# Kernel optimization log

Hardware: AMD Instinct MI355X
Metric: run time of the kernel (lower is better)

Reference implementation:

```python
import jax, jax.numpy as jnp
import numpy as np

DIM = 1024
HEADS = 16
HEAD_DIM = DIM // HEADS
THRESH = 0.29514
SHARP = 15.0
LN_EPS = 1e-5
NORM_EPS = 1e-12


def setup_inputs() -> dict:
    key = jax.random.key(0)
    ks = jax.random.split(key, 8)
    s = 1.0 / np.sqrt(DIM)
    sg = 1.0 / np.sqrt(HEAD_DIM)
    return {
        "x": jax.random.normal(ks[0], (2, 2048, DIM), dtype=jnp.float32),
        "Wq": jax.random.uniform(ks[1], (DIM, DIM), jnp.float32, -s, s),
        "Wk": jax.random.uniform(ks[2], (DIM, DIM), jnp.float32, -s, s),
        "Wv": jax.random.uniform(ks[3], (DIM, DIM), jnp.float32, -s, s),
        "gq": jax.random.uniform(ks[4], (HEAD_DIM,), jnp.float32, -sg, sg),
        "gk": jax.random.uniform(ks[5], (HEAD_DIM,), jnp.float32, -sg, sg),
        "Wo": jax.random.uniform(ks[6], (DIM, DIM), jnp.float32, -s, s),
        "bo": jax.random.uniform(ks[7], (DIM,), jnp.float32, -s, s),
        "ln_w": jnp.ones((DIM,), jnp.float32),
        "ln_b": jnp.zeros((DIM,), jnp.float32),
    }


def _l2norm(t):
    # F.normalize: t / max(||t||_2, eps)
    n = jnp.sqrt(jnp.sum(t * t, axis=-1, keepdims=True))
    return t / jnp.maximum(n, NORM_EPS)


def reference(x, Wq, Wk, Wv, gq, gk, Wo, bo, ln_w, ln_b):
    B, T, D = x.shape
    # LayerNorm over last dim
    mu = jnp.mean(x, axis=-1, keepdims=True)
    var = jnp.mean((x - mu) ** 2, axis=-1, keepdims=True)
    x_norm = (x - mu) / jnp.sqrt(var + LN_EPS) * ln_w + ln_b

    def split_heads(t):  # [B,T,D] -> [B,H,T,hd]
        return t.reshape(B, T, HEADS, HEAD_DIM).transpose(0, 2, 1, 3)

    q = _l2norm(split_heads(x_norm @ Wq))
    k = _l2norm(split_heads(x_norm @ Wk))
    v = split_heads(x @ Wv)  # note: v uses un-normalized x, as in source

    align = jnp.einsum("bhtd,bhsd->bhts", q, k)  # cosine alignment
    resonance = jax.nn.sigmoid((align - THRESH) * SHARP)
    gate_q = jnp.einsum("bhtd,d->bht", q, gq)
    gate_k = jnp.einsum("bhsd,d->bhs", k, gk)
    modulation = resonance * gate_q[..., :, None] * gate_k[..., None, :]
    collapse = jnp.einsum("bhts,bhsd->bhtd", modulation, v)
    collapse = collapse.transpose(0, 2, 1, 3).reshape(B, T, D)
    return collapse @ Wo + bo
```

## Files before the change

kernel.cpp:

```cpp
#include <hip/hip_runtime.h>
#include <math.h>

#define DIM 1024
#define T_SEQ 2048
#define NBATCH 2
#define HEADS 16
#define HD 64
#define NTOK 4096
#define THRESH 0.29514f
#define SHARP 15.0f
#define LOG2E 1.4426950408889634f

typedef __attribute__((ext_vector_type(8))) short bf16x8;
typedef __attribute__((ext_vector_type(4))) float f32x4;
typedef __attribute__((ext_vector_type(4))) unsigned int u32x4;

__device__ __forceinline__ unsigned short f2b(float f) {
    unsigned int u = __float_as_uint(f);
    unsigned int r = (u + 0x7FFFu + ((u >> 16) & 1u)) >> 16;
    return (unsigned short)r;
}
__device__ __forceinline__ float b2f(unsigned short u) {
    return __uint_as_float(((unsigned int)u) << 16);
}
__device__ __forceinline__ unsigned int pack2_bf16(float lo, float hi) {
    unsigned int a = __float_as_uint(lo) + 0x8000u;
    unsigned int b = __float_as_uint(hi) + 0x8000u;
    return __builtin_amdgcn_perm(b, a, 0x07060302u);
}

__device__ __forceinline__ void async_cp16(const unsigned short* g, unsigned short* l) {
    __builtin_amdgcn_global_load_lds(
        (const __attribute__((address_space(1))) unsigned int*)g,
        (__attribute__((address_space(3))) unsigned int*)l, 16, 0, 0);
}

__global__ __launch_bounds__(256) void ln_xnorm_kernel(
    const float* __restrict__ x, const float* __restrict__ lnw, const float* __restrict__ lnb,
    unsigned short* __restrict__ xnb, unsigned short* __restrict__ xb) {
    int row = blockIdx.x * 4 + (threadIdx.x >> 6);
    int lane = threadIdx.x & 63;
    const float4* xr = (const float4*)(x + (size_t)row * DIM);
    float4 v[4];
    float s = 0.f, ss = 0.f;
#pragma unroll
    for (int i = 0; i < 4; i++) {
        v[i] = xr[lane + i * 64];
        s += v[i].x + v[i].y + v[i].z + v[i].w;
        ss += v[i].x * v[i].x + v[i].y * v[i].y + v[i].z * v[i].z + v[i].w * v[i].w;
    }
#pragma unroll
    for (int off = 32; off; off >>= 1) {
        s += __shfl_xor(s, off);
        ss += __shfl_xor(ss, off);
    }
    float m = s * (1.f / DIM);
    float rstd = rsqrtf(ss * (1.f / DIM) - m * m + 1e-5f);
#pragma unroll
    for (int i = 0; i < 4; i++) {
        int e = (lane + i * 64) * 4;
        float4 lw = *(const float4*)&lnw[e];
        float4 lb = *(const float4*)&lnb[e];
        ushort4 un, ur;
        un.x = f2b((v[i].x - m) * rstd * lw.x + lb.x);
        un.y = f2b((v[i].y - m) * rstd * lw.y + lb.y);
        un.z = f2b((v[i].z - m) * rstd * lw.z + lb.z);
        un.w = f2b((v[i].w - m) * rstd * lw.w + lb.w);
        ur.x = f2b(v[i].x); ur.y = f2b(v[i].y); ur.z = f2b(v[i].z); ur.w = f2b(v[i].w);
        *(ushort4*)&xnb[(size_t)row * DIM + e] = un;
        *(ushort4*)&xb[(size_t)row * DIM + e] = ur;
    }
}

__global__ __launch_bounds__(256) void wtrans_kernel(
    const float* __restrict__ W0, const float* __restrict__ W1,
    const float* __restrict__ W2, const float* __restrict__ W3,
    unsigned short* __restrict__ T0, unsigned short* __restrict__ T1,
    unsigned short* __restrict__ T2, unsigned short* __restrict__ T3) {
    __shared__ float tile[64][65];
    const int z = blockIdx.z;
    const float* W = (z == 0) ? W0 : (z == 1) ? W1 : (z == 2) ? W2 : W3;
    unsigned short* T = (z == 0) ? T0 : (z == 1) ? T1 : (z == 2) ? T2 : T3;
    const int k0 = blockIdx.x * 64, n0 = blockIdx.y * 64;
    const int r = threadIdx.x >> 3;
    const int c = (threadIdx.x & 7) * 8;
#pragma unroll
    for (int half = 0; half < 2; half++) {
        int rr = r + half * 32;
        float4 a = *(const float4*)&W[(size_t)(k0 + rr) * DIM + n0 + c];
        float4 b = *(const float4*)&W[(size_t)(k0 + rr) * DIM + n0 + c + 4];
        tile[rr][c + 0] = a.x; tile[rr][c + 1] = a.y; tile[rr][c + 2] = a.z; tile[rr][c + 3] = a.w;
        tile[rr][c + 4] = b.x; tile[rr][c + 5] = b.y; tile[rr][c + 6] = b.z; tile[rr][c + 7] = b.w;
    }
    __syncthreads();
#pragma unroll
    for (int half = 0; half < 2; half++) {
        int dd = r + half * 32;
        bf16x8 o;
#pragma unroll
        for (int j = 0; j < 8; j++) o[j] = (short)f2b(tile[c + j][dd]);
        *(bf16x8*)&T[(size_t)(n0 + dd) * DIM + k0 + c] = o;
    }
}

template <int MODE>
__global__ __launch_bounds__(256) void gemm_mfma_kernel(
    const unsigned short* __restrict__ A0, const unsigned short* __restrict__ A2,
    const unsigned short* __restrict__ Bt0, const unsigned short* __restrict__ Bt1,
    const unsigned short* __restrict__ Bt2, const float* __restrict__ bias,
    const float* __restrict__ gq, const float* __restrict__ gk,
    unsigned short* __restrict__ Oq, unsigned short* __restrict__ Ok,
    unsigned short* __restrict__ Ov, float* __restrict__ gq_t, float* __restrict__ gk_t,
    float* __restrict__ Oout) {
    __shared__ __align__(16) unsigned short As[128 * 32];
    __shared__ __align__(16) unsigned short Bs[128 * 32];
    const int tid = threadIdx.x;
    const int lane = tid & 63, w = tid >> 6;
    const int l16 = lane & 15, quad = lane >> 4;
    const int wm = w >> 1, wn = w & 1;
    const int m0 = blockIdx.x * 128, n0 = blockIdx.y * 128;
    const unsigned short* A;
    const unsigned short* Bt;
    int z = 0;
    if constexpr (MODE == 0) {
        z = blockIdx.z;
        A = (z == 2) ? A2 : A0;
        Bt = (z == 0) ? Bt0 : (z == 1) ? Bt1 : Bt2;
    } else {
        A = A0;
        Bt = Bt0;
    }
    f32x4 acc[4][4] = {};
    const int kswz = (l16 >> 1) & 3;

    for (int k0 = 0; k0 < DIM; k0 += 32) {
        __syncthreads();
#pragma unroll
        for (int i = 0; i < 2; i++) {
            int linear = i * 256 + tid;
            int m = linear >> 2, kgp = linear & 3;
            int kgl = kgp ^ ((m >> 1) & 3);
            async_cp16(A + (size_t)(m0 + m) * DIM + k0 + kgl * 8, As + linear * 8);
            async_cp16(Bt + (size_t)(n0 + m) * DIM + k0 + kgl * 8, Bs + linear * 8);
        }
        __syncthreads();
        bf16x8 af[4], bfr[4];
#pragma unroll
        for (int t = 0; t < 4; t++) {
            int ma = wm * 64 + t * 16 + l16;
            af[t] = *(const bf16x8*)(As + ma * 32 + ((quad ^ kswz) * 8));
            int nb = wn * 64 + t * 16 + l16;
            bfr[t] = *(const bf16x8*)(Bs + nb * 32 + ((quad ^ kswz) * 8));
        }
#pragma unroll
        for (int mt = 0; mt < 4; mt++)
#pragma unroll
            for (int nt = 0; nt < 4; nt++)
                acc[mt][nt] =
                    __builtin_amdgcn_mfma_f32_16x16x32_bf16(af[mt], bfr[nt], acc[mt][nt], 0, 0, 0);
    }

    if constexpr (MODE == 0) {
        const int h = (n0 + wn * 64) >> 6;
        if (z <= 1) {
            constexpr float QSCALE = -SHARP * LOG2E;
            const float* gvec = (z == 0) ? gq : gk;
            float* gate = (z == 0) ? gq_t : gk_t;
            unsigned short* O = (z == 0) ? Oq : Ok;
            const float oscale = (z == 0) ? QSCALE : 1.0f;
            float gv[4];
#pragma unroll
            for (int nt = 0; nt < 4; nt++) gv[nt] = gvec[nt * 16 + l16];
#pragma unroll
            for (int mt = 0; mt < 4; mt++) {
#pragma unroll
                for (int r = 0; r < 4; r++) {
                    float ss = 0.f;
#pragma unroll
                    for (int nt = 0; nt < 4; nt++) ss += acc[mt][nt][r] * acc[mt][nt][r];
#pragma unroll
                    for (int msk = 1; msk < 16; msk <<= 1) ss += __shfl_xor(ss, msk);
                    float rn = __builtin_amdgcn_rcpf(fmaxf(sqrtf(ss), 1e-12f));
                    float vn[4], gg = 0.f;
#pragma unroll
                    for (int nt = 0; nt < 4; nt++) {
                        vn[nt] = acc[mt][nt][r] * rn;
                        gg += vn[nt] * gv[nt];
                    }
#pragma unroll
                    for (int msk = 1; msk < 16; msk <<= 1) gg += __shfl_xor(gg, msk);
                    int tok = m0 + wm * 64 + mt * 16 + quad * 4 + r;
                    int b = tok >> 11, t = tok & 2047;
                    size_t rowbase = ((size_t)(b * HEADS + h) * T_SEQ + t) * HD;
#pragma unroll
                    for (int nt = 0; nt < 4; nt++)
                        O[rowbase + nt * 16 + l16] = f2b(vn[nt] * oscale);
                    if (l16 == 0) gate[(b * HEADS + h) * T_SEQ + t] = gg;
                }
            }
        } else {
#pragma unroll
            for (int mt = 0; mt < 4; mt++) {
#pragma unroll
                for (int r = 0; r < 4; r++) {
                    int tok = m0 + wm * 64 + mt * 16 + quad * 4 + r;
                    int b = tok >> 11, t = tok & 2047;
                    size_t rowbase = ((size_t)(b * HEADS + h) * T_SEQ + t) * HD;
#pragma unroll
                    for (int nt = 0; nt < 4; nt++)
                        Ov[rowbase + nt * 16 + l16] = f2b(acc[mt][nt][r]);
                }
            }
        }
    } else {
        float bias_r[4];
#pragma unroll
        for (int nt = 0; nt < 4; nt++) bias_r[nt] = bias[n0 + wn * 64 + nt * 16 + l16];
#pragma unroll
        for (int mt = 0; mt < 4; mt++) {
#pragma unroll
            for (int r = 0; r < 4; r++) {
                int tok = m0 + wm * 64 + mt * 16 + quad * 4 + r;
#pragma unroll
                for (int nt = 0; nt < 4; nt++) {
                    int n = n0 + wn * 64 + nt * 16 + l16;
                    Oout[(size_t)tok * DIM + n] = acc[mt][nt][r] + bias_r[nt];
                }
            }
        }
    }
}

__global__ __launch_bounds__(256) void vtrans_kernel(const unsigned short* __restrict__ Vn,
                                                     const float* __restrict__ gk_t,
                                                     unsigned short* __restrict__ Vt) {
    __shared__ float tile[64][65];
    const int bh = blockIdx.y;
    const int t0 = blockIdx.x * 64;
    const int r = threadIdx.x >> 3;
    const int c = (threadIdx.x & 7) * 8;
    const unsigned short* src = Vn + (size_t)bh * T_SEQ * HD;
#pragma unroll
    for (int half = 0; half < 2; half++) {
        int rr = r + half * 32;
        float gkv = gk_t[bh * T_SEQ + t0 + rr];
        bf16x8 v = *(const bf16x8*)(src + (size_t)(t0 + rr) * HD + c);
#pragma unroll
        for (int j = 0; j < 8; j++) tile[rr][c + j] = b2f((unsigned short)v[j]) * gkv;
    }
    __syncthreads();
    unsigned short* dst = Vt + (size_t)bh * HD * T_SEQ;
#pragma unroll
    for (int half = 0; half < 2; half++) {
        int dd = r + half * 32;
        bf16x8 o;
#pragma unroll
        for (int j = 0; j < 8; j++) o[j] = (short)f2b(tile[c + j][dd]);
        *(bf16x8*)(dst + (size_t)dd * T_SEQ + t0 + c) = o;
    }
}

__global__ __launch_bounds__(256, 4) void attn_mfma_kernel(
    const unsigned short* __restrict__ Qn, const unsigned short* __restrict__ Kn,
    const unsigned short* __restrict__ Vt, const float* __restrict__ gateq,
    unsigned short* __restrict__ collp0, unsigned short* __restrict__ collp1) {
    __shared__ __align__(16) unsigned short Ks[2][64 * 64];
    __shared__ __align__(16) unsigned short VtL[2][64 * 64];
    const int tid = threadIdx.x;
    const int lane = tid & 63, w = tid >> 6;
    const int quad = lane >> 4, l16 = lane & 15;
    const int t0 = blockIdx.x * 128;
    const int h = blockIdx.y;
    const int zz = blockIdx.z;
    const int b = zz >> 1, shalf = zz & 1;
    const int sbase = shalf * (T_SEQ / 2);
    const int bh = b * HEADS + h;
    const size_t base = (size_t)bh * T_SEQ * HD;
    constexpr float K0 = THRESH * SHARP * LOG2E;
    const f32x4 k0v = {K0, K0, K0, K0};

    int det0 = quad, det1 = quad + 4;
    asm("v_permlane16_swap_b32 %0, %1" : "+v"(det0), "+v"(det1));
    const bool flagA = (__builtin_amdgcn_readfirstlane(det0) == 0);

    bf16x8 fq[2][2];
#pragma unroll
    for (int mt = 0; mt < 2; mt++) {
        const unsigned short* qrow = Qn + base + (size_t)(t0 + w * 32 + mt * 16 + l16) * HD;
        fq[mt][0] = *(const bf16x8*)(qrow + quad * 8);
        fq[mt][1] = *(const bf16x8*)(qrow + 32 + quad * 8);
    }

    f32x4 oacc[4][2] = {};
    const int srow = tid >> 3;
    const int sgp = tid & 7;
    const int swz = l16 & 7;

    auto stage_chunk = [&](unsigned short* ksn, unsigned short* vtn, int s0) {
#pragma unroll
        for (int half = 0; half < 2; half++) {
            int row = srow + half * 32;
            int g = sgp ^ (row & 7);
            async_cp16(Kn + base + (size_t)(s0 + row) * HD + g * 8, ksn + row * 64 + sgp * 8);
            async_cp16(Vt + base + (size_t)row * T_SEQ + s0 + g * 8, vtn + row * 64 + sgp * 8);
        }
    };

    auto do_chunk = [&](const unsigned short* ksb, const unsigned short* vtb) {
#pragma unroll
        for (int kh = 0; kh < 2; kh++) {
            unsigned int p[2][2][2];
#pragma unroll
            for (int ct2 = 0; ct2 < 2; ct2++) {
                const int ct = 2 * kh + ct2;
                const unsigned short* krow = ksb + (ct * 16 + l16) * 64;
                bf16x8 fk0 = *(const bf16x8*)(krow + (quad ^ swz) * 8);
                bf16x8 fk1 = *(const bf16x8*)(krow + ((quad + 4) ^ swz) * 8);
#pragma unroll
                for (int mt = 0; mt < 2; mt++) {
                    __builtin_amdgcn_s_setprio(1);
                    f32x4 s1 =
                        __builtin_amdgcn_mfma_f32_16x16x32_bf16(fk0, fq[mt][0], k0v, 0, 0, 0);
                    f32x4 sacc =
                        __builtin_amdgcn_mfma_f32_16x16x32_bf16(fk1, fq[mt][1], s1, 0, 0, 0);
                    __builtin_amdgcn_s_setprio(0);
                    float w0 = __builtin_amdgcn_rcpf(1.f + __builtin_amdgcn_exp2f(sacc[0]));
                    float w1 = __builtin_amdgcn_rcpf(1.f + __builtin_amdgcn_exp2f(sacc[1]));
                    float w2 = __builtin_amdgcn_rcpf(1.f + __builtin_amdgcn_exp2f(sacc[2]));
                    float w3 = __builtin_amdgcn_rcpf(1.f + __builtin_amdgcn_exp2f(sacc[3]));
                    p[mt][ct2][0] = pack2_bf16(w0, w1);
                    p[mt][ct2][1] = pack2_bf16(w2, w3);
                }
            }
            int gv = (4 * kh + 2 * (quad & 1) + (quad >> 1)) ^ swz;
            bf16x8 fv[4];
#pragma unroll
            for (int dt = 0; dt < 4; dt++)
                fv[dt] = *(const bf16x8*)(vtb + (dt * 16 + l16) * 64 + gv * 8);
#pragma unroll
            for (int mt = 0; mt < 2; mt++) {
                unsigned int aL = p[mt][0][0], aH = p[mt][0][1];
                unsigned int bL = p[mt][1][0], bH = p[mt][1][1];
                asm("v_permlane16_swap_b32 %0, %1" : "+v"(aL), "+v"(bL));
                asm("v_permlane16_swap_b32 %0, %1" : "+v"(aH), "+v"(bH));
                u32x4 bt;
                if (flagA) {
                    bt.x = aL; bt.y = aH; bt.z = bL; bt.w = bH;
                } else {
                    bt.x = bL; bt.y = bH; bt.z = aL; bt.w = aH;
                }
                bf16x8 fs = __builtin_bit_cast(bf16x8, bt);
                __builtin_amdgcn_s_setprio(1);
#pragma unroll
                for (int dt = 0; dt < 4; dt++)
                    oacc[dt][mt] =
                        __builtin_amdgcn_mfma_f32_16x16x32_bf16(fv[dt], fs, oacc[dt][mt], 0, 0, 0);
                __builtin_amdgcn_s_setprio(0);
            }
        }
        __syncthreads();
    };

    stage_chunk(&Ks[0][0], &VtL[0][0], sbase);
    __syncthreads();

    for (int j = 0; j < T_SEQ / 256; j++) {
        stage_chunk(&Ks[1][0], &VtL[1][0], sbase + j * 128 + 64);
        do_chunk(&Ks[0][0], &VtL[0][0]);
        if (j + 1 < T_SEQ / 256) stage_chunk(&Ks[0][0], &VtL[0][0], sbase + j * 128 + 128);
        do_chunk(&Ks[1][0], &VtL[1][0]);
    }

    unsigned short* collp = shalf ? collp1 : collp0;
#pragma unroll
    for (int mt = 0; mt < 2; mt++) {
        int t = t0 + w * 32 + mt * 16 + l16;
        float gq_v = gateq[bh * T_SEQ + t];
        unsigned short* dst = collp + ((size_t)b * T_SEQ + t) * DIM + h * HD;
#pragma unroll
        for (int dt = 0; dt < 4; dt++) {
            ushort4 o;
            o.x = f2b(oacc[dt][mt][0] * gq_v);
            o.y = f2b(oacc[dt][mt][1] * gq_v);
            o.z = f2b(oacc[dt][mt][2] * gq_v);
            o.w = f2b(oacc[dt][mt][3] * gq_v);
            *(ushort4*)(dst + dt * 16 + quad * 4) = o;
        }
    }
}

__global__ __launch_bounds__(256) void merge_kernel(unsigned short* __restrict__ p0,
                                                    const unsigned short* __restrict__ p1) {
    size_t i = ((size_t)blockIdx.x * 256 + threadIdx.x) * 8;
    bf16x8 a = *(const bf16x8*)(p0 + i);
    bf16x8 c = *(const bf16x8*)(p1 + i);
    bf16x8 o;
#pragma unroll
    for (int j = 0; j < 8; j++)
        o[j] = (short)f2b(b2f((unsigned short)a[j]) + b2f((unsigned short)c[j]));
    *(bf16x8*)(p0 + i) = o;
}

extern "C" void kernel_launch(void* const* d_in, const int* in_sizes, int n_in,
                              void* d_out, int out_size, void* d_ws, size_t ws_size,
                              hipStream_t stream) {
    const float* x = (const float*)d_in[0];
    const float* Wq = (const float*)d_in[1];
    const float* Wk = (const float*)d_in[2];
    const float* Wv = (const float*)d_in[3];
    const float* gq = (const float*)d_in[4];
    const float* gk = (const float*)d_in[5];
    const float* Wo = (const float*)d_in[6];
    const float* bo = (const float*)d_in[7];
    const float* lnw = (const float*)d_in[8];
    const float* lnb = (const float*)d_in[9];
    float* out = (float*)d_out;

    unsigned short* ws = (unsigned short*)d_ws;
    unsigned short* xnb = ws;
    unsigned short* xb = xnb + (size_t)NTOK * DIM;
    unsigned short* Wqt = xb + (size_t)NTOK * DIM;
    unsigned short* Wkt = Wqt + (size_t)DIM * DIM;
    unsigned short* Wvt = Wkt + (size_t)DIM * DIM;
    unsigned short* Wot = Wvt + (size_t)DIM * DIM;
    unsigned short* Q16 = Wot + (size_t)DIM * DIM;
    unsigned short* K16 = Q16 + (size_t)NTOK * DIM;
    unsigned short* Vn = K16 + (size_t)NTOK * DIM;
    float* gq_t = (float*)(Vn + (size_t)NTOK * DIM);
    float* gk_t = gq_t + NBATCH * HEADS * T_SEQ;
    unsigned short* collb1 = (unsigned short*)(gk_t + NBATCH * HEADS * T_SEQ);
    unsigned short* Vt = xnb;
    unsigned short* collb0 = xb;

    ln_xnorm_kernel<<<NTOK / 4, 256, 0, stream>>>(x, lnw, lnb, xnb, xb);
    wtrans_kernel<<<dim3(16, 16, 4), 256, 0, stream>>>(Wq, Wk, Wv, Wo, Wqt, Wkt, Wvt, Wot);
    gemm_mfma_kernel<0><<<dim3(NTOK / 128, DIM / 128, 3), 256, 0, stream>>>(
        xnb, xb, Wqt, Wkt, Wvt, nullptr, gq, gk, Q16, K16, Vn, gq_t, gk_t, nullptr);
    vtrans_kernel<<<dim3(T_SEQ / 64, NBATCH * HEADS), 256, 0, stream>>>(Vn, gk_t, Vt);
    attn_mfma_kernel<<<dim3(T_SEQ / 128, HEADS, NBATCH * 2), 256, 0, stream>>>(
        Q16, K16, Vt, gq_t, collb0, collb1);
    merge_kernel<<<(NTOK * DIM) / (256 * 8), 256, 0, stream>>>(collb0, collb1);
    gemm_mfma_kernel<1><<<dim3(NTOK / 128, DIM / 128, 1), 256, 0, stream>>>(
        collb0, nullptr, Wot, nullptr, nullptr, bo, nullptr, nullptr, nullptr, nullptr, nullptr,
        nullptr, nullptr, out);
}
```

Before: 220.8 us.

## Halve attention query tile per block and remap block IDs for XCD locality

Each attention block now handles 64 query rows instead of 128, one 16-row M-tile per wave, which doubles the grid to 2048 blocks. Block indices are remapped so that blocks placed on the same XCD (round-robin by 8) share the same (b, h, s-half) K/V stream, aiming for better L2 reuse. The smaller tile halves per-wave accumulator and Q registers and may raise occupancy. In exchange, each K/V chunk staged in LDS is reused by half as many query rows, so total K/V loads and LDS traffic per unit of work double.

```diff
diff --git a/kernel.cpp b/kernel.cpp
--- a/kernel.cpp
+++ b/kernel.cpp
@@ -269,9 +269,11 @@
     const int tid = threadIdx.x;
     const int lane = tid & 63, w = tid >> 6;
     const int quad = lane >> 4, l16 = lane & 15;
-    const int t0 = blockIdx.x * 128;
-    const int h = blockIdx.y;
-    const int zz = blockIdx.z;
+    const int f = blockIdx.x + 32 * blockIdx.y + 512 * blockIdx.z;
+    const int work = (f & 7) * 256 + (f >> 3);
+    const int t0 = (work & 31) * 64;
+    const int h = (work >> 5) & 15;
+    const int zz = work >> 9;
     const int b = zz >> 1, shalf = zz & 1;
     const int sbase = shalf * (T_SEQ / 2);
     const int bh = b * HEADS + h;
@@ -283,15 +285,14 @@
     asm("v_permlane16_swap_b32 %0, %1" : "+v"(det0), "+v"(det1));
     const bool flagA = (__builtin_amdgcn_readfirstlane(det0) == 0);
 
-    bf16x8 fq[2][2];
-#pragma unroll
-    for (int mt = 0; mt < 2; mt++) {
-        const unsigned short* qrow = Qn + base + (size_t)(t0 + w * 32 + mt * 16 + l16) * HD;
-        fq[mt][0] = *(const bf16x8*)(qrow + quad * 8);
-        fq[mt][1] = *(const bf16x8*)(qrow + 32 + quad * 8);
-    }
-
-    f32x4 oacc[4][2] = {};
+    bf16x8 fq[2];
+    {
+        const unsigned short* qrow = Qn + base + (size_t)(t0 + w * 16 + l16) * HD;
+        fq[0] = *(const bf16x8*)(qrow + quad * 8);
+        fq[1] = *(const bf16x8*)(qrow + 32 + quad * 8);
+    }
+
+    f32x4 oacc[4] = {};
     const int srow = tid >> 3;
     const int sgp = tid & 7;
     const int swz = l16 & 7;
@@ -309,54 +310,45 @@
     auto do_chunk = [&](const unsigned short* ksb, const unsigned short* vtb) {
 #pragma unroll
         for (int kh = 0; kh < 2; kh++) {
-            unsigned int p[2][2][2];
+            unsigned int p[2][2];
 #pragma unroll
             for (int ct2 = 0; ct2 < 2; ct2++) {
                 const int ct = 2 * kh + ct2;
                 const unsigned short* krow = ksb + (ct * 16 + l16) * 64;
                 bf16x8 fk0 = *(const bf16x8*)(krow + (quad ^ swz) * 8);
                 bf16x8 fk1 = *(const bf16x8*)(krow + ((quad + 4) ^ swz) * 8);
-#pragma unroll
-                for (int mt = 0; mt < 2; mt++) {
-                    __builtin_amdgcn_s_setprio(1);
-                    f32x4 s1 =
-                        __builtin_amdgcn_mfma_f32_16x16x32_bf16(fk0, fq[mt][0], k0v, 0, 0, 0);
-                    f32x4 sacc =
-                        __builtin_amdgcn_mfma_f32_16x16x32_bf16(fk1, fq[mt][1], s1, 0, 0, 0);
-                    __builtin_amdgcn_s_setprio(0);
-                    float w0 = __builtin_amdgcn_rcpf(1.f + __builtin_amdgcn_exp2f(sacc[0]));
-                    float w1 = __builtin_amdgcn_rcpf(1.f + __builtin_amdgcn_exp2f(sacc[1]));
-                    float w2 = __builtin_amdgcn_rcpf(1.f + __builtin_amdgcn_exp2f(sacc[2]));
-                    float w3 = __builtin_amdgcn_rcpf(1.f + __builtin_amdgcn_exp2f(sacc[3]));
-                    p[mt][ct2][0] = pack2_bf16(w0, w1);
-                    p[mt][ct2][1] = pack2_bf16(w2, w3);
-                }
+                __builtin_amdgcn_s_setprio(1);
+                f32x4 s1 = __builtin_amdgcn_mfma_f32_16x16x32_bf16(fk0, fq[0], k0v, 0, 0, 0);
+                f32x4 sacc = __builtin_amdgcn_mfma_f32_16x16x32_bf16(fk1, fq[1], s1, 0, 0, 0);
+                __builtin_amdgcn_s_setprio(0);
+                float w0 = __builtin_amdgcn_rcpf(1.f + __builtin_amdgcn_exp2f(sacc[0]));
+                float w1 = __builtin_amdgcn_rcpf(1.f + __builtin_amdgcn_exp2f(sacc[1]));
+                float w2 = __builtin_amdgcn_rcpf(1.f + __builtin_amdgcn_exp2f(sacc[2]));
+                float w3 = __builtin_amdgcn_rcpf(1.f + __builtin_amdgcn_exp2f(sacc[3]));
+                p[ct2][0] = pack2_bf16(w0, w1);
+                p[ct2][1] = pack2_bf16(w2, w3);
             }
             int gv = (4 * kh + 2 * (quad & 1) + (quad >> 1)) ^ swz;
             bf16x8 fv[4];
 #pragma unroll
             for (int dt = 0; dt < 4; dt++)
                 fv[dt] = *(const bf16x8*)(vtb + (dt * 16 + l16) * 64 + gv * 8);
-#pragma unroll
-            for (int mt = 0; mt < 2; mt++) {
-                unsigned int aL = p[mt][0][0], aH = p[mt][0][1];
-                unsigned int bL = p[mt][1][0], bH = p[mt][1][1];
-                asm("v_permlane16_swap_b32 %0, %1" : "+v"(aL), "+v"(bL));
-                asm("v_permlane16_swap_b32 %0, %1" : "+v"(aH), "+v"(bH));
-                u32x4 bt;
-                if (flagA) {
-                    bt.x = aL; bt.y = aH; bt.z = bL; bt.w = bH;
-                } else {
-                    bt.x = bL; bt.y = bH; bt.z = aL; bt.w = aH;
-                }
-                bf16x8 fs = __builtin_bit_cast(bf16x8, bt);
-                __builtin_amdgcn_s_setprio(1);
-#pragma unroll
-                for (int dt = 0; dt < 4; dt++)
-                    oacc[dt][mt] =
-                        __builtin_amdgcn_mfma_f32_16x16x32_bf16(fv[dt], fs, oacc[dt][mt], 0, 0, 0);
-                __builtin_amdgcn_s_setprio(0);
+            unsigned int aL = p[0][0], aH = p[0][1];
+            unsigned int bL = p[1][0], bH = p[1][1];
+            asm("v_permlane16_swap_b32 %0, %1" : "+v"(aL), "+v"(bL));
+            asm("v_permlane16_swap_b32 %0, %1" : "+v"(aH), "+v"(bH));
+            u32x4 bt;
+            if (flagA) {
+                bt.x = aL; bt.y = aH; bt.z = bL; bt.w = bH;
+            } else {
+                bt.x = bL; bt.y = bH; bt.z = aL; bt.w = aH;
             }
+            bf16x8 fs = __builtin_bit_cast(bf16x8, bt);
+            __builtin_amdgcn_s_setprio(1);
+#pragma unroll
+            for (int dt = 0; dt < 4; dt++)
+                oacc[dt] = __builtin_amdgcn_mfma_f32_16x16x32_bf16(fv[dt], fs, oacc[dt], 0, 0, 0);
+            __builtin_amdgcn_s_setprio(0);
         }
         __syncthreads();
     };
@@ -372,18 +364,17 @@
     }
 
     unsigned short* collp = shalf ? collp1 : collp0;
-#pragma unroll
-    for (int mt = 0; mt < 2; mt++) {
-        int t = t0 + w * 32 + mt * 16 + l16;
+    {
+        int t = t0 + w * 16 + l16;
         float gq_v = gateq[bh * T_SEQ + t];
         unsigned short* dst = collp + ((size_t)b * T_SEQ + t) * DIM + h * HD;
 #pragma unroll
         for (int dt = 0; dt < 4; dt++) {
             ushort4 o;
-            o.x = f2b(oacc[dt][mt][0] * gq_v);
-            o.y = f2b(oacc[dt][mt][1] * gq_v);
-            o.z = f2b(oacc[dt][mt][2] * gq_v);
-            o.w = f2b(oacc[dt][mt][3] * gq_v);
+            o.x = f2b(oacc[dt][0] * gq_v);
+            o.y = f2b(oacc[dt][1] * gq_v);
+            o.z = f2b(oacc[dt][2] * gq_v);
+            o.w = f2b(oacc[dt][3] * gq_v);
             *(ushort4*)(dst + dt * 16 + quad * 4) = o;
         }
     }
@@ -437,7 +428,7 @@
     gemm_mfma_kernel<0><<<dim3(NTOK / 128, DIM / 128, 3), 256, 0, stream>>>(
         xnb, xb, Wqt, Wkt, Wvt, nullptr, gq, gk, Q16, K16, Vn, gq_t, gk_t, nullptr);
     vtrans_kernel<<<dim3(T_SEQ / 64, NBATCH * HEADS), 256, 0, stream>>>(Vn, gk_t, Vt);
-    attn_mfma_kernel<<<dim3(T_SEQ / 128, HEADS, NBATCH * 2), 256, 0, stream>>>(
+    attn_mfma_kernel<<<dim3(T_SEQ / 64, HEADS, NBATCH * 2), 256, 0, stream>>>(
         Q16, K16, Vt, gq_t, collb0, collb1);
     merge_kernel<<<(NTOK * DIM) / (256 * 8), 256, 0, stream>>>(collb0, collb1);
     gemm_mfma_kernel<1><<<dim3(NTOK / 128, DIM / 128, 1), 256, 0, stream>>>(
```

Result: no change. 223.3 us (+1.1%).
